# Kernel optimization log

Measured on AMD Instinct MI355X. Metric: run time of the kernel, lower is better.

The kernel has to match this reference:

```python
import jax, jax.numpy as jnp
import numpy as np

DIM = 384
HEADS = 12
WS = 7
MLPH = 1536
B = 32
EPS = 1e-5


def _rel_index():
    coords = np.stack(np.meshgrid(np.arange(WS), np.arange(WS), indexing='ij'))  # [2,7,7]
    cf = coords.reshape(2, -1)  # [2,49]
    rel = cf[:, :, None] - cf[:, None, :]  # [2,49,49]
    rel = rel.transpose(1, 2, 0).astype(np.int64)
    rel[:, :, 0] += WS - 1
    rel[:, :, 1] += WS - 1
    rel[:, :, 0] *= 2 * WS - 1
    return jnp.asarray(rel.sum(-1), dtype=jnp.int32)  # [49,49]


def setup_inputs() -> dict:
    key = jax.random.key(0)
    ks = jax.random.split(key, 16)
    H, W = 56, 56
    L = H * W
    s = 0.02
    inp = {
        'x': jax.random.normal(ks[0], (B, L, DIM), jnp.float32),
        'ln1_g': jnp.ones((DIM,), jnp.float32),
        'ln1_b': jnp.zeros((DIM,), jnp.float32),
        'qkv_w': jax.random.normal(ks[1], (DIM, 3 * DIM), jnp.float32) * s,
        'qkv_b': jnp.zeros((3 * DIM,), jnp.float32),
        'rpb_table': jax.random.normal(ks[2], ((2 * WS - 1) ** 2, HEADS), jnp.float32) * s,
        'proj_w': jax.random.normal(ks[3], (DIM, DIM), jnp.float32) * s,
        'proj_b': jnp.zeros((DIM,), jnp.float32),
        'ln2_g': jnp.ones((DIM,), jnp.float32),
        'ln2_b': jnp.zeros((DIM,), jnp.float32),
        'mlp_w1': jax.random.normal(ks[4], (DIM, MLPH), jnp.float32) * s,
        'mlp_b1': jnp.zeros((MLPH,), jnp.float32),
        'mlp_w2': jax.random.normal(ks[5], (MLPH, DIM), jnp.float32) * s,
        'mlp_b2': jnp.zeros((DIM,), jnp.float32),
        'rel_idx': _rel_index(),
        'H': H,
        'W': W,
    }
    return inp


def _ln(x, g, b):
    m = jnp.mean(x, axis=-1, keepdims=True)
    v = jnp.mean(jnp.square(x - m), axis=-1, keepdims=True)
    return (x - m) * jax.lax.rsqrt(v + EPS) * g + b


def reference(x, ln1_g, ln1_b, qkv_w, qkv_b, rpb_table, proj_w, proj_b,
              ln2_g, ln2_b, mlp_w1, mlp_b1, mlp_w2, mlp_b2, rel_idx, H, W):
    Bb, L, C = x.shape
    N = WS * WS
    hd = C // HEADS
    scale = hd ** -0.5

    shortcut = x
    h = _ln(x, ln1_g, ln1_b).reshape(Bb, H, W, C)
    # window partition -> [nW, 49, C]
    h = h.reshape(Bb, H // WS, WS, W // WS, WS, C).transpose(0, 1, 3, 2, 4, 5)
    wins = h.reshape(-1, N, C)
    nW = wins.shape[0]

    qkv = (wins @ qkv_w + qkv_b).reshape(nW, N, 3, HEADS, hd).transpose(2, 0, 3, 1, 4)
    q, k, v = qkv[0] * scale, qkv[1], qkv[2]  # [nW, heads, 49, hd]

    attn = jnp.einsum('bhnd,bhmd->bhnm', q, k)
    bias = rpb_table[rel_idx].transpose(2, 0, 1)  # [heads,49,49]
    attn = jax.nn.softmax(attn + bias[None], axis=-1)
    out = jnp.einsum('bhnm,bhmd->bhnd', attn, v).transpose(0, 2, 1, 3).reshape(nW, N, C)
    out = out @ proj_w + proj_b

    # window reverse -> [B, L, C]
    out = out.reshape(Bb, H // WS, W // WS, WS, WS, C).transpose(0, 1, 3, 2, 4, 5).reshape(Bb, L, C)

    x = shortcut + out
    h2 = _ln(x, ln2_g, ln2_b)
    mlp = jax.nn.gelu(h2 @ mlp_w1 + mlp_b1, approximate=False) @ mlp_w2 + mlp_b2
    return x + mlp
```

## Files before the change

kernel.cpp:

```cpp
#include <hip/hip_runtime.h>
#include <hip/hip_bf16.h>
#include <cstdint>
#include <cstddef>

#define HEADS 12
#define LL 3136
#define ROWS 100352
#define SCALE 0.17677669529663687f

typedef __hip_bfloat16 bf16;
typedef __attribute__((ext_vector_type(8))) short short8;
typedef __attribute__((ext_vector_type(4))) short s4;
typedef __attribute__((ext_vector_type(4))) float f32x4;

__device__ __forceinline__ float bf2f(unsigned short u) {
  union { uint32_t u32; float f; } x; x.u32 = ((uint32_t)u) << 16; return x.f;
}
__device__ __forceinline__ unsigned short f2bf_bits(float f) {
  union { float f; uint32_t u; } x; x.f = f;
  uint32_t r = x.u + 0x7fffu + ((x.u >> 16) & 1u);
  return (unsigned short)(r >> 16);
}
__device__ __forceinline__ float gelu_fast(float x) {
  float t2 = x * (1.5957691216f + 0.0713548162726f * x * x);
  float e = __expf(t2);
  return x * (e / (e + 1.0f));
}

__global__ __launch_bounds__(64) void prep_fragB(const float* __restrict__ src,
    bf16* __restrict__ dst, int K, int N, int scaleLim, float scale) {
  const int nf = blockIdx.x, kf = blockIdx.y;
  const int l = threadIdx.x;
  const int n = nf * 16 + (l & 15);
  const int k0 = kf * 32 + (l >> 4) * 8;
  const float sc = (n < scaleLim) ? scale : 1.f;
  short8 v;
  #pragma unroll
  for (int j = 0; j < 8; ++j)
    v[j] = (short)f2bf_bits(src[(size_t)(k0 + j) * N + n] * sc);
  *(short8*)&dst[(((size_t)nf * (K >> 5) + kf) * 64 + l) * 8] = v;
}

__global__ void prep_qb(const float* __restrict__ qkv_b, float* __restrict__ qb) {
  int idx = blockIdx.x * 256 + threadIdx.x;
  if (idx < 1152) qb[idx] = qkv_b[idx] * (idx < 384 ? SCALE : 1.0f);
}

__global__ void prep_biasM(const float* __restrict__ rpb, const int* __restrict__ rel,
                           f32x4* __restrict__ biasM) {
  int h = blockIdx.x;
  int t = blockIdx.y;
  int mi = t >> 2, ni = t & 3;
  int lane = threadIdx.x;
  int q = ni * 16 + (lane & 15);
  int g = lane >> 4;
  f32x4 v;
  #pragma unroll
  for (int j = 0; j < 4; ++j) {
    int k = mi * 16 + g * 4 + j;
    float b;
    if (k < 49) b = (q < 49) ? rpb[rel[q * 49 + k] * HEADS + h] : 0.f;
    else        b = -1e30f;
    v[j] = b;
  }
  biasM[((h * 4 + mi) * 4 + ni) * 64 + lane] = v;
}

template<bool WIN, bool BF16IN>
__global__ __launch_bounds__(256) void ln_kernel(const float* __restrict__ xf,
    const bf16* __restrict__ xb, const float* __restrict__ g,
    const float* __restrict__ b, bf16* __restrict__ out) {
  int row = blockIdx.x * 4 + (threadIdx.x >> 6);
  int lane = threadIdx.x & 63;
  size_t src;
  if (WIN) {
    int w = row / 49, p = row - w * 49;
    int bb = w >> 6, wy = (w >> 3) & 7, wx = w & 7;
    int iy = p / 7, ix = p - iy * 7;
    int l = (wy * 7 + iy) * 56 + wx * 7 + ix;
    src = ((size_t)bb * LL + l) * 384;
  } else {
    src = (size_t)row * 384;
  }
  float vals[6];
  float s = 0.f, s2 = 0.f;
  #pragma unroll
  for (int j = 0; j < 6; ++j) {
    float v = BF16IN ? bf2f(*(const unsigned short*)&xb[src + lane + 64 * j])
                     : xf[src + lane + 64 * j];
    vals[j] = v; s += v; s2 += v * v;
  }
  #pragma unroll
  for (int off = 32; off >= 1; off >>= 1) {
    s  += __shfl_xor(s, off);
    s2 += __shfl_xor(s2, off);
  }
  float m  = s * (1.f / 384.f);
  float var = s2 * (1.f / 384.f) - m * m;
  float rs = rsqrtf(var + 1e-5f);
  bf16* orow = out + (size_t)row * 384;
  #pragma unroll
  for (int j = 0; j < 6; ++j) {
    int c = lane + 64 * j;
    orow[c] = __float2bfloat16((vals[j] - m) * rs * g[c] + b[c]);
  }
}

template<int EPI, int KTOT>
__global__ __launch_bounds__(256) void gemm_bt(const bf16* __restrict__ A,
    const bf16* __restrict__ Bt, const float* __restrict__ bias,
    bf16* __restrict__ Cb, float* __restrict__ Cf, const float* __restrict__ resid,
    const bf16* __restrict__ residb, int M, int N) {
  constexpr int NKF = KTOT >> 5;
  constexpr int NT  = KTOT >> 5;
  __shared__ bf16 lsA[2][128 * 32];
  const int t = threadIdx.x;
  const int lane = t & 63;
  const int wave = t >> 6;
  const int wm = wave >> 1, wn = wave & 1;
  const int lrow = lane & 15;
  const int lk = (lane >> 4) * 8;
  const int nbx = N >> 7;
  const int nwg = (M >> 7) * nbx;
  const int cpx = nwg >> 3;
  const int id2 = (blockIdx.x & 7) * cpx + (blockIdx.x >> 3);
  const int n0 = (id2 % nbx) * 128;
  const int m0 = (id2 / nbx) * 128;

  f32x4 acc[4][4];
  #pragma unroll
  for (int i = 0; i < 4; ++i)
    #pragma unroll
    for (int j = 0; j < 4; ++j) acc[i][j] = (f32x4){0.f, 0.f, 0.f, 0.f};

  const int e0 = t * 8;
  const int r0 = e0 >> 5, c0s = e0 & 31;
  const bf16* aptr0 = A + (size_t)(m0 + r0) * KTOT + c0s;
  const int e1 = (256 + t) * 8;
  const int r1 = e1 >> 5, c1s = e1 & 31;
  const bf16* aptr1 = A + (size_t)(m0 + r1) * KTOT + c1s;
  const bf16* fb = Bt + (((size_t)((n0 >> 4) + wn * 4) * NKF) * 64 + lane) * 8;

  auto stageA = [&](int buf, int tile) {
    __builtin_amdgcn_global_load_lds(
        (const __attribute__((address_space(1))) void*)(aptr0 + tile * 32),
        (__attribute__((address_space(3))) void*)&lsA[buf][e0], 16, 0, 0);
    __builtin_amdgcn_global_load_lds(
        (const __attribute__((address_space(1))) void*)(aptr1 + tile * 32),
        (__attribute__((address_space(3))) void*)&lsA[buf][e1], 16, 0, 0);
  };

  auto loadB = [&](int kf, short8 (&dst)[4]) {
    const bf16* p = fb + kf * 512;
    #pragma unroll
    for (int ni = 0; ni < 4; ++ni)
      dst[ni] = *(const short8*)(p + (size_t)ni * NKF * 512);
  };

  auto computeA = [&](int buf, const short8 (&bfr)[4]) {
    short8 af[4];
    #pragma unroll
    for (int mi = 0; mi < 4; ++mi)
      af[mi] = *(const short8*)&lsA[buf][(wm * 64 + mi * 16 + lrow) * 32 + lk];
    #pragma unroll
    for (int mi = 0; mi < 4; ++mi)
      #pragma unroll
      for (int ni = 0; ni < 4; ++ni)
        acc[mi][ni] = __builtin_amdgcn_mfma_f32_16x16x32_bf16(af[mi], bfr[ni], acc[mi][ni], 0, 0, 0);
  };

  short8 b0[4], b1[4];
  stageA(0, 0);
  loadB(0, b0);
  __syncthreads();
  #pragma unroll 2
  for (int it = 0; it < NT; it += 2) {
    if (it + 1 < NT) {
      stageA(1, it + 1);
      loadB(it + 1, b1);
    }
    computeA(0, b0);
    __syncthreads();
    if (it + 1 < NT) {
      if (it + 2 < NT) {
        stageA(0, it + 2);
        loadB(it + 2, b0);
      }
      computeA(1, b1);
      __syncthreads();
    }
  }

  #pragma unroll
  for (int mi = 0; mi < 4; ++mi) {
    #pragma unroll
    for (int ni = 0; ni < 4; ++ni) {
      int col = n0 + wn * 64 + ni * 16 + lrow;
      float bv = bias[col];
      #pragma unroll
      for (int j = 0; j < 4; ++j) {
        int row = m0 + wm * 64 + mi * 16 + (lane >> 4) * 4 + j;
        float v = acc[mi][ni][j] + bv;
        if constexpr (EPI == 0) {
          Cb[(size_t)row * N + col] = __float2bfloat16(v);
        } else if constexpr (EPI == 1) {
          Cb[(size_t)row * N + col] = __float2bfloat16(gelu_fast(v));
        } else if constexpr (EPI == 2) {
          int w = row / 49, p = row - w * 49;
          int bb = w >> 6, wy = (w >> 3) & 7, wx = w & 7;
          int iy = p / 7, ix = p - iy * 7;
          int l = (wy * 7 + iy) * 56 + wx * 7 + ix;
          size_t di = ((size_t)bb * LL + l) * 384 + col;
          Cb[di] = __float2bfloat16(v + resid[di]);
        } else {
          size_t di = (size_t)row * N + col;
          Cf[di] = v + bf2f(*(const unsigned short*)&residb[di]);
        }
      }
    }
  }
}

__global__ __launch_bounds__(256) void attn_mfma(const bf16* __restrict__ qkv,
    const f32x4* __restrict__ biasM, bf16* __restrict__ out) {
  __shared__ __align__(16) short lds4[4][6272];
  const int wv = threadIdx.x >> 6;
  const int lane = threadIdx.x & 63;
  const int w = blockIdx.x * 4 + wv;
  const int h = blockIdx.y;
  short* L = &lds4[wv][0];
  const short* base = (const short*)(qkv + (size_t)w * 49 * 1152 + h * 32);

  #pragma unroll
  for (int i = 0; i < 4; ++i) {
    int t = i * 64 + lane;
    int r = t >> 2, c = t & 3;
    short8 qv, kv, vv;
    if (r < 49) {
      const short* rp = base + (size_t)r * 1152;
      qv = *(const short8*)(rp + c * 8);
      kv = *(const short8*)(rp + 384 + c * 8);
      vv = *(const short8*)(rp + 768 + c * 8);
    } else {
      qv = (short8)0; kv = (short8)0; vv = (short8)0;
    }
    *(short8*)&L[r * 32 + c * 8] = kv;
    *(short8*)&L[2048 + r * 32 + c * 8] = qv;
    #pragma unroll
    for (int j = 0; j < 8; ++j) L[4096 + (c * 8 + j) * 68 + r] = vv[j];
  }

  const int g = lane >> 4, r15 = lane & 15;

  short8 ka[4], qb[4];
  #pragma unroll
  for (int mi = 0; mi < 4; ++mi)
    ka[mi] = *(const short8*)&L[(mi * 16 + r15) * 32 + g * 8];
  #pragma unroll
  for (int ni = 0; ni < 4; ++ni)
    qb[ni] = *(const short8*)&L[2048 + (ni * 16 + r15) * 32 + g * 8];

  f32x4 sT[4][4];
  #pragma unroll
  for (int mi = 0; mi < 4; ++mi)
    #pragma unroll
    for (int ni = 0; ni < 4; ++ni)
      sT[mi][ni] = biasM[((h * 4 + mi) * 4 + ni) * 64 + lane];
  #pragma unroll
  for (int mi = 0; mi < 4; ++mi)
    #pragma unroll
    for (int ni = 0; ni < 4; ++ni)
      sT[mi][ni] = __builtin_amdgcn_mfma_f32_16x16x32_bf16(ka[mi], qb[ni], sT[mi][ni], 0, 0, 0);

  float inv_[4];
  #pragma unroll
  for (int ni = 0; ni < 4; ++ni) {
    float m = -1e30f;
    #pragma unroll
    for (int mi = 0; mi < 4; ++mi)
      #pragma unroll
      for (int j = 0; j < 4; ++j) m = fmaxf(m, sT[mi][ni][j]);
    m = fmaxf(m, __shfl_xor(m, 16));
    m = fmaxf(m, __shfl_xor(m, 32));
    float s = 0.f;
    #pragma unroll
    for (int mi = 0; mi < 4; ++mi)
      #pragma unroll
      for (int j = 0; j < 4; ++j) {
        float p = __expf(sT[mi][ni][j] - m);
        sT[mi][ni][j] = p; s += p;
      }
    s += __shfl_xor(s, 16);
    s += __shfl_xor(s, 32);
    inv_[ni] = 1.f / s;
  }

  s4 pa[4][4];
  #pragma unroll
  for (int mi = 0; mi < 4; ++mi)
    #pragma unroll
    for (int ni = 0; ni < 4; ++ni) {
      s4 p;
      #pragma unroll
      for (int j = 0; j < 4; ++j)
        p[j] = (short)f2bf_bits(sT[mi][ni][j] * inv_[ni]);
      pa[mi][ni] = p;
    }

  s4 vb[4][2];
  #pragma unroll
  for (int mi = 0; mi < 4; ++mi)
    #pragma unroll
    for (int di = 0; di < 2; ++di)
      vb[mi][di] = *(const s4*)&L[4096 + (di * 16 + r15) * 68 + mi * 16 + g * 4];

  f32x4 o[4][2];
  #pragma unroll
  for (int ni = 0; ni < 4; ++ni)
    #pragma unroll
    for (int di = 0; di < 2; ++di) o[ni][di] = (f32x4){0.f, 0.f, 0.f, 0.f};

  asm volatile("s_nop 3" ::: );
  #pragma unroll
  for (int ni = 0; ni < 4; ++ni)
    #pragma unroll
    for (int di = 0; di < 2; ++di)
      #pragma unroll
      for (int mi = 0; mi < 4; ++mi) {
#if __has_builtin(__builtin_amdgcn_mfma_f32_16x16x16bf16_1k)
        o[ni][di] = __builtin_amdgcn_mfma_f32_16x16x16bf16_1k(pa[mi][ni], vb[mi][di], o[ni][di], 0, 0, 0);
#else
        asm volatile("v_mfma_f32_16x16x16_bf16 %0, %1, %2, %0"
                     : "+v"(o[ni][di]) : "v"(pa[mi][ni]), "v"(vb[mi][di]));
#endif
      }
  asm volatile("s_nop 7\n\ts_nop 7" ::: );

  bf16* op = out + ((size_t)w * 49) * 384 + h * 32;
  #pragma unroll
  for (int ni = 0; ni < 4; ++ni)
    #pragma unroll
    for (int di = 0; di < 2; ++di)
      #pragma unroll
      for (int j = 0; j < 4; ++j) {
        int q = ni * 16 + g * 4 + j;
        if (q < 49)
          op[(size_t)q * 384 + di * 16 + r15] = __float2bfloat16(o[ni][di][j]);
      }
}

extern "C" void kernel_launch(void* const* d_in, const int* in_sizes, int n_in,
                              void* d_out, int out_size, void* d_ws, size_t ws_size,
                              hipStream_t stream) {
  const float* x      = (const float*)d_in[0];
  const float* ln1_g  = (const float*)d_in[1];
  const float* ln1_b  = (const float*)d_in[2];
  const float* qkv_w  = (const float*)d_in[3];
  const float* qkv_b  = (const float*)d_in[4];
  const float* rpb    = (const float*)d_in[5];
  const float* proj_w = (const float*)d_in[6];
  const float* proj_b = (const float*)d_in[7];
  const float* ln2_g  = (const float*)d_in[8];
  const float* ln2_b  = (const float*)d_in[9];
  const float* mlp_w1 = (const float*)d_in[10];
  const float* mlp_b1 = (const float*)d_in[11];
  const float* mlp_w2 = (const float*)d_in[12];
  const float* mlp_b2 = (const float*)d_in[13];
  const int*   rel    = (const int*)d_in[14];

  char* ws = (char*)d_ws;
  const size_t OFF_WQKV  = 0;
  const size_t OFF_WPROJ = OFF_WQKV + (size_t)1152 * 384 * 2;
  const size_t OFF_WM1   = OFF_WPROJ + (size_t)384 * 384 * 2;
  const size_t OFF_WM2   = OFF_WM1 + (size_t)1536 * 384 * 2;
  const size_t OFF_QB    = OFF_WM2 + (size_t)384 * 1536 * 2;
  const size_t OFF_HWIN  = 3659776;
  const size_t OFF_QKV   = OFF_HWIN + (size_t)ROWS * 384 * 2;
  const size_t OFF_ATTN  = OFF_QKV + (size_t)ROWS * 1152 * 2;
  const size_t OFF_X2    = OFF_ATTN + (size_t)ROWS * 384 * 2;
  const size_t OFF_M1    = OFF_QKV;
  const size_t OFF_H2    = OFF_HWIN;
  const size_t OFF_BIASM = OFF_X2 + (size_t)ROWS * 384 * 2;

  bf16*  wqkv  = (bf16*)(ws + OFF_WQKV);
  bf16*  wproj = (bf16*)(ws + OFF_WPROJ);
  bf16*  wm1   = (bf16*)(ws + OFF_WM1);
  bf16*  wm2   = (bf16*)(ws + OFF_WM2);
  float* qb    = (float*)(ws + OFF_QB);
  f32x4* biasM = (f32x4*)(ws + OFF_BIASM);
  bf16*  hwin  = (bf16*)(ws + OFF_HWIN);
  bf16*  qkvb  = (bf16*)(ws + OFF_QKV);
  bf16*  attnb = (bf16*)(ws + OFF_ATTN);
  bf16*  x2b   = (bf16*)(ws + OFF_X2);
  bf16*  m1    = (bf16*)(ws + OFF_M1);
  bf16*  h2    = (bf16*)(ws + OFF_H2);
  float* outp  = (float*)d_out;

  prep_fragB<<<dim3(1152 / 16, 384 / 32), 64, 0, stream>>>(qkv_w, wqkv, 384, 1152, 384, SCALE);
  prep_fragB<<<dim3(384 / 16, 384 / 32), 64, 0, stream>>>(proj_w, wproj, 384, 384, 0, 1.f);
  prep_fragB<<<dim3(1536 / 16, 384 / 32), 64, 0, stream>>>(mlp_w1, wm1, 384, 1536, 0, 1.f);
  prep_fragB<<<dim3(384 / 16, 1536 / 32), 64, 0, stream>>>(mlp_w2, wm2, 1536, 384, 0, 1.f);
  prep_qb<<<5, 256, 0, stream>>>(qkv_b, qb);
  prep_biasM<<<dim3(12, 16), 64, 0, stream>>>(rpb, rel, biasM);

  ln_kernel<true, false><<<ROWS / 4, 256, 0, stream>>>(x, nullptr, ln1_g, ln1_b, hwin);
  gemm_bt<0, 384><<<(1152 / 128) * (ROWS / 128), 256, 0, stream>>>(
      hwin, wqkv, qb, qkvb, nullptr, nullptr, nullptr, ROWS, 1152);
  attn_mfma<<<dim3(512, HEADS), 256, 0, stream>>>(qkvb, biasM, attnb);
  gemm_bt<2, 384><<<(384 / 128) * (ROWS / 128), 256, 0, stream>>>(
      attnb, wproj, proj_b, x2b, nullptr, x, nullptr, ROWS, 384);
  ln_kernel<false, true><<<ROWS / 4, 256, 0, stream>>>(nullptr, x2b, ln2_g, ln2_b, h2);
  gemm_bt<1, 384><<<(1536 / 128) * (ROWS / 128), 256, 0, stream>>>(
      h2, wm1, mlp_b1, m1, nullptr, nullptr, nullptr, ROWS, 1536);
  gemm_bt<3, 1536><<<(384 / 128) * (ROWS / 128), 256, 0, stream>>>(
      m1, wm2, mlp_b2, nullptr, outp, nullptr, x2b, ROWS, 384);
}
```

Baseline: 932.4 us.

## Fuse MLP up-projection, GELU and down-projection into one kernel

Replaces the two MLP GEMMs with one kernel. Each 64-row tile keeps its LN2 output in LDS, computes 128-column chunks of the hidden layer with GELU into LDS, and accumulates the down-projection in registers, so the 1536-wide hidden activation never goes to global memory. LN2 now writes its output in the MFMA fragment layout so the fused kernel can load it straight into LDS with global_load_lds. The cost is that weights are read from global/L2 for every 64-row tile, each wave holds 24 accumulator fragments, and the 58KB of LDS per block limits occupancy.

```diff
diff --git a/kernel.cpp b/kernel.cpp
--- a/kernel.cpp
+++ b/kernel.cpp
@@ -25,6 +25,10 @@
   float t2 = x * (1.5957691216f + 0.0713548162726f * x * x);
   float e = __expf(t2);
   return x * (e / (e + 1.0f));
+}
+__device__ __forceinline__ size_t frag_addr(int row, int c, int nkf) {
+  return ((size_t)(row >> 4) * nkf + (c >> 5)) * 512
+       + (size_t)(((row & 15) + (((c & 31) >> 3) << 4)) * 8 + (c & 7));
 }
 
 __global__ __launch_bounds__(64) void prep_fragB(const float* __restrict__ src,
@@ -66,7 +70,7 @@
   biasM[((h * 4 + mi) * 4 + ni) * 64 + lane] = v;
 }
 
-template<bool WIN, bool BF16IN>
+template<bool WIN, bool BF16IN, bool FRAGOUT>
 __global__ __launch_bounds__(256) void ln_kernel(const float* __restrict__ xf,
     const bf16* __restrict__ xb, const float* __restrict__ g,
     const float* __restrict__ b, bf16* __restrict__ out) {
@@ -98,11 +102,12 @@
   float m  = s * (1.f / 384.f);
   float var = s2 * (1.f / 384.f) - m * m;
   float rs = rsqrtf(var + 1e-5f);
-  bf16* orow = out + (size_t)row * 384;
   #pragma unroll
   for (int j = 0; j < 6; ++j) {
     int c = lane + 64 * j;
-    orow[c] = __float2bfloat16((vals[j] - m) * rs * g[c] + b[c]);
+    float v = (vals[j] - m) * rs * g[c] + b[c];
+    if (FRAGOUT) out[frag_addr(row, c, 12)] = __float2bfloat16(v);
+    else         out[(size_t)row * 384 + c] = __float2bfloat16(v);
   }
 }
 
@@ -203,8 +208,6 @@
         float v = acc[mi][ni][j] + bv;
         if constexpr (EPI == 0) {
           Cb[(size_t)row * N + col] = __float2bfloat16(v);
-        } else if constexpr (EPI == 1) {
-          Cb[(size_t)row * N + col] = __float2bfloat16(gelu_fast(v));
         } else if constexpr (EPI == 2) {
           int w = row / 49, p = row - w * 49;
           int bb = w >> 6, wy = (w >> 3) & 7, wx = w & 7;
@@ -212,13 +215,119 @@
           int l = (wy * 7 + iy) * 56 + wx * 7 + ix;
           size_t di = ((size_t)bb * LL + l) * 384 + col;
           Cb[di] = __float2bfloat16(v + resid[di]);
-        } else {
-          size_t di = (size_t)row * N + col;
-          Cf[di] = v + bf2f(*(const unsigned short*)&residb[di]);
         }
       }
     }
   }
+}
+
+__global__ __launch_bounds__(256) void mlp_fused(const bf16* __restrict__ Af,
+    const bf16* __restrict__ W1f, const bf16* __restrict__ W2f,
+    const float* __restrict__ b1, const float* __restrict__ b2,
+    const bf16* __restrict__ residb, float* __restrict__ outp) {
+  __shared__ bf16 lsA[64 * 384];
+  __shared__ bf16 lsM[64 * 128];
+  const int t = threadIdx.x;
+  const int lane = t & 63;
+  const int wave = t >> 6;
+  const int wm = wave >> 1, wn = wave & 1;
+  const int g = lane >> 4, r15 = lane & 15;
+  const int nwg = ROWS / 64;
+  const int cpx = nwg >> 3;
+  const int blk = (blockIdx.x & 7) * cpx + (blockIdx.x >> 3);
+  const int m0 = blk * 64;
+
+  const bf16* srcA = Af + (size_t)(m0 >> 4) * 12 * 512;
+  #pragma unroll
+  for (int i = 0; i < 12; ++i) {
+    int e = (i * 256 + t) * 8;
+    __builtin_amdgcn_global_load_lds(
+        (const __attribute__((address_space(1))) void*)(srcA + e),
+        (__attribute__((address_space(3))) void*)&lsA[e], 16, 0, 0);
+  }
+
+  f32x4 acc2[2][12];
+  #pragma unroll
+  for (int i = 0; i < 2; ++i)
+    #pragma unroll
+    for (int j = 0; j < 12; ++j) acc2[i][j] = (f32x4){0.f, 0.f, 0.f, 0.f};
+
+  __syncthreads();
+
+  for (int c = 0; c < 12; ++c) {
+    f32x4 acc1[2][4];
+    #pragma unroll
+    for (int i = 0; i < 2; ++i)
+      #pragma unroll
+      for (int j = 0; j < 4; ++j) acc1[i][j] = (f32x4){0.f, 0.f, 0.f, 0.f};
+    const int nfb1 = c * 8 + wn * 4;
+    #pragma unroll
+    for (int ks = 0; ks < 12; ++ks) {
+      short8 af[2];
+      #pragma unroll
+      for (int mi = 0; mi < 2; ++mi) {
+        int rf = wm * 2 + mi;
+        af[mi] = *(const short8*)&lsA[((rf * 12 + ks) * 64 + lane) * 8];
+      }
+      short8 bf1[4];
+      #pragma unroll
+      for (int ni = 0; ni < 4; ++ni)
+        bf1[ni] = *(const short8*)&W1f[(((size_t)(nfb1 + ni) * 12 + ks) * 64 + lane) * 8];
+      #pragma unroll
+      for (int mi = 0; mi < 2; ++mi)
+        #pragma unroll
+        for (int ni = 0; ni < 4; ++ni)
+          acc1[mi][ni] = __builtin_amdgcn_mfma_f32_16x16x32_bf16(af[mi], bf1[ni], acc1[mi][ni], 0, 0, 0);
+    }
+    __syncthreads();
+    #pragma unroll
+    for (int mi = 0; mi < 2; ++mi)
+      #pragma unroll
+      for (int ni = 0; ni < 4; ++ni) {
+        int ccol = wn * 64 + ni * 16 + r15;
+        float bv = b1[c * 128 + ccol];
+        #pragma unroll
+        for (int j = 0; j < 4; ++j) {
+          int r = wm * 32 + mi * 16 + g * 4 + j;
+          float v = gelu_fast(acc1[mi][ni][j] + bv);
+          size_t ad = ((size_t)(r >> 4) * 4 + (ccol >> 5)) * 512
+                    + (size_t)(((r & 15) + (((ccol & 31) >> 3) << 4)) * 8 + (ccol & 7));
+          lsM[ad] = __float2bfloat16(v);
+        }
+      }
+    __syncthreads();
+    #pragma unroll
+    for (int k2 = 0; k2 < 4; ++k2) {
+      short8 af2[2];
+      #pragma unroll
+      for (int mi = 0; mi < 2; ++mi) {
+        int rf = wm * 2 + mi;
+        af2[mi] = *(const short8*)&lsM[((rf * 4 + k2) * 64 + lane) * 8];
+      }
+      const int kf2 = c * 4 + k2;
+      #pragma unroll
+      for (int ni = 0; ni < 12; ++ni) {
+        short8 bf2 = *(const short8*)&W2f[(((size_t)(wn * 12 + ni) * 48 + kf2) * 64 + lane) * 8];
+        #pragma unroll
+        for (int mi = 0; mi < 2; ++mi)
+          acc2[mi][ni] = __builtin_amdgcn_mfma_f32_16x16x32_bf16(af2[mi], bf2, acc2[mi][ni], 0, 0, 0);
+      }
+    }
+  }
+
+  #pragma unroll
+  for (int mi = 0; mi < 2; ++mi)
+    #pragma unroll
+    for (int ni = 0; ni < 12; ++ni) {
+      int col = wn * 192 + ni * 16 + r15;
+      float bv = b2[col];
+      #pragma unroll
+      for (int j = 0; j < 4; ++j) {
+        int row = m0 + wm * 32 + mi * 16 + g * 4 + j;
+        size_t di = (size_t)row * 384 + col;
+        outp[di] = acc2[mi][ni][j] + bv + bf2f(*(const unsigned short*)&residb[di]);
+      }
+    }
 }
 
 __global__ __launch_bounds__(256) void attn_mfma(const bf16* __restrict__ qkv,
@@ -378,7 +487,6 @@
   const size_t OFF_QKV   = OFF_HWIN + (size_t)ROWS * 384 * 2;
   const size_t OFF_ATTN  = OFF_QKV + (size_t)ROWS * 1152 * 2;
   const size_t OFF_X2    = OFF_ATTN + (size_t)ROWS * 384 * 2;
-  const size_t OFF_M1    = OFF_QKV;
   const size_t OFF_H2    = OFF_HWIN;
   const size_t OFF_BIASM = OFF_X2 + (size_t)ROWS * 384 * 2;
 
@@ -392,7 +500,6 @@
   bf16*  qkvb  = (bf16*)(ws + OFF_QKV);
   bf16*  attnb = (bf16*)(ws + OFF_ATTN);
   bf16*  x2b   = (bf16*)(ws + OFF_X2);
-  bf16*  m1    = (bf16*)(ws + OFF_M1);
   bf16*  h2    = (bf16*)(ws + OFF_H2);
   float* outp  = (float*)d_out;
 
@@ -403,15 +510,12 @@
   prep_qb<<<5, 256, 0, stream>>>(qkv_b, qb);
   prep_biasM<<<dim3(12, 16), 64, 0, stream>>>(rpb, rel, biasM);
 
-  ln_kernel<true, false><<<ROWS / 4, 256, 0, stream>>>(x, nullptr, ln1_g, ln1_b, hwin);
+  ln_kernel<true, false, false><<<ROWS / 4, 256, 0, stream>>>(x, nullptr, ln1_g, ln1_b, hwin);
   gemm_bt<0, 384><<<(1152 / 128) * (ROWS / 128), 256, 0, stream>>>(
       hwin, wqkv, qb, qkvb, nullptr, nullptr, nullptr, ROWS, 1152);
   attn_mfma<<<dim3(512, HEADS), 256, 0, stream>>>(qkvb, biasM, attnb);
   gemm_bt<2, 384><<<(384 / 128) * (ROWS / 128), 256, 0, stream>>>(
       attnb, wproj, proj_b, x2b, nullptr, x, nullptr, ROWS, 384);
-  ln_kernel<false, true><<<ROWS / 4, 256, 0, stream>>>(nullptr, x2b, ln2_g, ln2_b, h2);
-  gemm_bt<1, 384><<<(1536 / 128) * (ROWS / 128), 256, 0, stream>>>(
-      h2, wm1, mlp_b1, m1, nullptr, nullptr, nullptr, ROWS, 1536);
-  gemm_bt<3, 1536><<<(384 / 128) * (ROWS / 128), 256, 0, stream>>>(
-      m1, wm2, mlp_b2, nullptr, outp, nullptr, x2b, ROWS, 384);
-}
+  ln_kernel<false, true, true><<<ROWS / 4, 256, 0, stream>>>(nullptr, x2b, ln2_g, ln2_b, h2);
+  mlp_fused<<<ROWS / 64, 256, 0, stream>>>(h2, wm1, wm2, mlp_b1, mlp_b2, x2b, outp);
+}
```

New measurement: 2.252 ms. +141.6%, slower.
